# Kernel optimization log

Measured on AMD Instinct MI355X. Metric: run time of the kernel, lower is better.

The kernel has to match this reference:

```python
import jax, jax.numpy as jnp
import numpy as np

D, H, FF, EPS = 1024, 16, 4096, 1e-5

def _ln(x, g, b):
    m = jnp.mean(x, axis=-1, keepdims=True)
    v = jnp.var(x, axis=-1, keepdims=True)
    return (x - m) * jax.lax.rsqrt(v + EPS) * g + b

def setup_inputs() -> dict:
    key = jax.random.key(0)
    ks = jax.random.split(key, 8)
    b, t = 2, 2048
    return {
        "x": jax.random.normal(ks[0], (b, t, D), jnp.float32),
        "prev_attn": jax.random.normal(ks[1], (b, H, t, t), jnp.float32) * 0.1,
        "w_qkv": jax.random.normal(ks[2], (D, 3 * D), jnp.float32) * (D ** -0.5),
        "w_out": jax.random.normal(ks[3], (D, D), jnp.float32) * (D ** -0.5),
        "w1": jax.random.normal(ks[4], (D, FF), jnp.float32) * (D ** -0.5),
        "b1": jnp.zeros((FF,), jnp.float32),
        "w2": jax.random.normal(ks[5], (FF, D), jnp.float32) * (FF ** -0.5),
        "b2": jnp.zeros((D,), jnp.float32),
        "g1": jnp.ones((D,), jnp.float32),
        "be1": jnp.zeros((D,), jnp.float32),
        "g2": jnp.ones((D,), jnp.float32),
        "be2": jnp.zeros((D,), jnp.float32),
    }

def reference(x, prev_attn, w_qkv, w_out, w1, b1, w2, b2, g1, be1, g2, be2):
    b, t, d = x.shape
    h, hd = H, d // H
    scale = hd ** -0.5
    qkv = _ln(x, g1, be1) @ w_qkv                       # [b,t,3d]
    q, k, v = jnp.split(qkv, 3, axis=-1)
    q, k, v = [z.reshape(b, t, h, hd).transpose(0, 2, 1, 3) for z in (q, k, v)]
    attn = jnp.einsum('bhid,bhjd->bhij', q, k) * scale + prev_attn
    attn = jax.nn.softmax(attn, axis=-1)                # [b,h,t,t]
    out = jnp.einsum('bhij,bhjd->bhid', attn, v).transpose(0, 2, 1, 3).reshape(b, t, d)
    x = x + out @ w_out
    hdn = _ln(x, g2, be2)
    ffn = jax.nn.gelu(hdn @ w1 + b1, approximate=False) @ w2 + b2
    x = x + ffn
    return (x, jax.lax.stop_gradient(attn))
```

## Files before the change

### kernel.cpp

```cpp
#include <hip/hip_runtime.h>
#include <hip/hip_bf16.h>
#include <math.h>

#define T_SEQ 2048
#define D_MODEL 1024
#define N_HEADS 16
#define HD 64
#define FF_DIM 4096
#define N_ROWS 4096
#define LDQKV 3072

typedef __bf16 bf16x8 __attribute__((ext_vector_type(8)));
typedef float f32x4 __attribute__((ext_vector_type(4)));

__device__ __forceinline__ unsigned short f2bf(float f) {
  union { float f; unsigned u; } v; v.f = f;
  unsigned r = v.u + 0x7FFFu + ((v.u >> 16) & 1u);
  return (unsigned short)(r >> 16);
}
__device__ __forceinline__ float bf2f(unsigned short u) {
  union { unsigned u; float f; } v; v.u = ((unsigned)u) << 16;
  return v.f;
}

__device__ __forceinline__ void gld_lds16(const void* g, void* l) {
  __builtin_amdgcn_global_load_lds(
      (const __attribute__((address_space(1))) unsigned int*)g,
      (__attribute__((address_space(3))) unsigned int*)l, 16, 0, 0);
}

__global__ __launch_bounds__(256) void transpose_w(const float* __restrict__ src,
                                                   unsigned short* __restrict__ dst,
                                                   int R, int C) {
  __shared__ float tile[32][33];
  int c0 = blockIdx.x * 32, r0 = blockIdx.y * 32;
  int tx = threadIdx.x & 31, ty = threadIdx.x >> 5;
#pragma unroll
  for (int i = 0; i < 32; i += 8)
    tile[ty + i][tx] = src[(size_t)(r0 + ty + i) * C + c0 + tx];
  __syncthreads();
#pragma unroll
  for (int i = 0; i < 32; i += 8)
    dst[(size_t)(c0 + ty + i) * R + r0 + tx] = f2bf(tile[tx][ty + i]);
}

__global__ __launch_bounds__(256) void ln_kernel(const float* __restrict__ x,
                                                 const float* __restrict__ g,
                                                 const float* __restrict__ be,
                                                 unsigned short* __restrict__ out) {
  int row = blockIdx.x;
  float4 v = ((const float4*)(x + (size_t)row * D_MODEL))[threadIdx.x];
  float s = v.x + v.y + v.z + v.w;
  float ss = v.x * v.x + v.y * v.y + v.z * v.z + v.w * v.w;
#pragma unroll
  for (int o = 32; o; o >>= 1) { s += __shfl_down(s, o); ss += __shfl_down(ss, o); }
  __shared__ float red[8];
  int wid = threadIdx.x >> 6, lane = threadIdx.x & 63;
  if (lane == 0) { red[wid] = s; red[4 + wid] = ss; }
  __syncthreads();
  if (threadIdx.x == 0) {
    float S0 = red[0] + red[1] + red[2] + red[3];
    float S1 = red[4] + red[5] + red[6] + red[7];
    float m = S0 * (1.0f / D_MODEL);
    red[0] = m;
    red[1] = rsqrtf(S1 * (1.0f / D_MODEL) - m * m + 1e-5f);
  }
  __syncthreads();
  float m = red[0], inv = red[1];
  float4 gv = ((const float4*)g)[threadIdx.x];
  float4 bv = ((const float4*)be)[threadIdx.x];
  ushort4 o;
  o.x = f2bf((v.x - m) * inv * gv.x + bv.x);
  o.y = f2bf((v.y - m) * inv * gv.y + bv.y);
  o.z = f2bf((v.z - m) * inv * gv.z + bv.z);
  o.w = f2bf((v.w - m) * inv * gv.w + bv.w);
  ((ushort4*)(out + (size_t)row * D_MODEL))[threadIdx.x] = o;
}

template <int EPI>
__global__ __launch_bounds__(256) void gemm_bt(const unsigned short* __restrict__ A,
                                               const unsigned short* __restrict__ Bt,
                                               int M, int N, int K,
                                               void* __restrict__ outp,
                                               const float* __restrict__ bias,
                                               const float* __restrict__ res) {
  __shared__ __align__(16) unsigned short As[128 * 32];
  __shared__ __align__(16) unsigned short Bs[128 * 32];
  int tid = threadIdx.x;
  int m0 = blockIdx.x * 128, n0 = blockIdx.y * 128;
  int w = tid >> 6, l = tid & 63;
  int wm = w >> 1, wn = w & 1;
  int lr = l & 15, lg = l >> 4;
  f32x4 acc[4][4] = {};
  const unsigned short* ap0 = A + (size_t)(m0 + (tid >> 2)) * K + (tid & 3) * 8;
  const unsigned short* ap1 = ap0 + (size_t)64 * K;
  const unsigned short* bp0 = Bt + (size_t)(n0 + (tid >> 2)) * K + (tid & 3) * 8;
  const unsigned short* bp1 = bp0 + (size_t)64 * K;
  unsigned short* la0 = As + (tid & ~63) * 8;
  unsigned short* la1 = As + (256 + (tid & ~63)) * 8;
  unsigned short* lb0 = Bs + (tid & ~63) * 8;
  unsigned short* lb1 = Bs + (256 + (tid & ~63)) * 8;
  for (int k0 = 0; k0 < K; k0 += 32) {
    gld_lds16(ap0, la0);
    gld_lds16(ap1, la1);
    gld_lds16(bp0, lb0);
    gld_lds16(bp1, lb1);
    ap0 += 32; ap1 += 32; bp0 += 32; bp1 += 32;
    __syncthreads();
    bf16x8 af[4], bfr[4];
#pragma unroll
    for (int i = 0; i < 4; i++) {
      af[i] = *(const bf16x8*)(As + (wm * 64 + i * 16 + lr) * 32 + lg * 8);
      bfr[i] = *(const bf16x8*)(Bs + (wn * 64 + i * 16 + lr) * 32 + lg * 8);
    }
#pragma unroll
    for (int i = 0; i < 4; i++)
#pragma unroll
      for (int j = 0; j < 4; j++)
        acc[i][j] = __builtin_amdgcn_mfma_f32_16x16x32_bf16(af[i], bfr[j], acc[i][j], 0, 0, 0);
    __syncthreads();
  }
#pragma unroll
  for (int i = 0; i < 4; i++) {
#pragma unroll
    for (int j = 0; j < 4; j++) {
      int col = n0 + wn * 64 + j * 16 + lr;
#pragma unroll
      for (int r = 0; r < 4; r++) {
        int row = m0 + wm * 64 + i * 16 + lg * 4 + r;
        size_t idx = (size_t)row * N + col;
        float v = acc[i][j][r];
        if (EPI == 0) {
          if (col < 1024) v *= 0.125f;
          ((unsigned short*)outp)[idx] = f2bf(v);
        } else if (EPI == 2) {
          float t = v + bias[col];
          ((unsigned short*)outp)[idx] = f2bf(0.5f * t * (1.0f + erff(t * 0.70710678f)));
        }
      }
    }
  }
}

template <int EPI>
__global__ __launch_bounds__(256) void gemm_bt2(const unsigned short* __restrict__ A,
                                                const unsigned short* __restrict__ Bt,
                                                int M, int N, int K,
                                                void* __restrict__ outp,
                                                const float* __restrict__ bias,
                                                const float* __restrict__ res) {
  __shared__ __align__(16) unsigned short As[64 * 64];
  __shared__ __align__(16) unsigned short Bs[128 * 64];
  int tid = threadIdx.x;
  int m0 = blockIdx.x * 64, n0 = blockIdx.y * 128;
  int w = tid >> 6, l = tid & 63;
  int lr = l & 15, lg = l >> 4;
  f32x4 acc[4][2] = {};
  int srow = tid >> 3;
  int scolb = ((tid & 7) * 16) ^ ((srow & 7) << 4);
  const unsigned short* apg = A + (size_t)(m0 + srow) * K + (scolb >> 1);
  const unsigned short* bpg = Bt + (size_t)(n0 + srow) * K + (scolb >> 1);
  unsigned short* la = As + tid * 8;
  unsigned short* lb = Bs + tid * 8;
  for (int k0 = 0; k0 < K; k0 += 64) {
    gld_lds16(apg + k0, la);
    gld_lds16(apg + (size_t)32 * K + k0, la + 32 * 64);
    gld_lds16(bpg + k0, lb);
    gld_lds16(bpg + (size_t)32 * K + k0, lb + 32 * 64);
    gld_lds16(bpg + (size_t)64 * K + k0, lb + 64 * 64);
    gld_lds16(bpg + (size_t)96 * K + k0, lb + 96 * 64);
    __syncthreads();
#pragma unroll
    for (int kk = 0; kk < 2; kk++) {
      int cb = (lg * 16 + kk * 64) ^ ((lr & 7) << 4);
      bf16x8 af[4], bfr[2];
#pragma unroll
      for (int i = 0; i < 4; i++)
        af[i] = *(const bf16x8*)((const char*)As + (i * 16 + lr) * 128 + cb);
#pragma unroll
      for (int j = 0; j < 2; j++)
        bfr[j] = *(const bf16x8*)((const char*)Bs + (w * 32 + j * 16 + lr) * 128 + cb);
#pragma unroll
      for (int i = 0; i < 4; i++)
#pragma unroll
        for (int j = 0; j < 2; j++)
          acc[i][j] = __builtin_amdgcn_mfma_f32_16x16x32_bf16(af[i], bfr[j], acc[i][j], 0, 0, 0);
    }
    __syncthreads();
  }
#pragma unroll
  for (int i = 0; i < 4; i++) {
#pragma unroll
    for (int j = 0; j < 2; j++) {
      int col = n0 + w * 32 + j * 16 + lr;
#pragma unroll
      for (int r = 0; r < 4; r++) {
        int row = m0 + i * 16 + lg * 4 + r;
        size_t idx = (size_t)row * N + col;
        float v = acc[i][j][r];
        if (EPI == 1) {
          ((float*)outp)[idx] = res[idx] + v;
        } else {
          ((float*)outp)[idx] = v + bias[col] + res[idx];
        }
      }
    }
  }
}

__global__ __launch_bounds__(256) void repack_kv(const unsigned short* __restrict__ qkv,
                                                 unsigned short* __restrict__ kt,
                                                 unsigned short* __restrict__ vt2) {
  __shared__ unsigned short tile[64][66];
  int bh = blockIdx.x >> 5, tt = blockIdx.x & 31;
  int b = bh >> 4, h = bh & 15;
  int t0 = tt * 64;
  int tid = threadIdx.x;
  const unsigned short* ksrc = qkv + (size_t)(b * T_SEQ + t0) * LDQKV + D_MODEL + h * HD;
  unsigned short* kdst = kt + ((size_t)bh * T_SEQ + t0) * HD;
#pragma unroll
  for (int i = 0; i < 16; i++) {
    int e = i * 256 + tid;
    int tr = e >> 6, d = e & 63;
    kdst[(size_t)tr * HD + d] = ksrc[(size_t)tr * LDQKV + d];
  }
  const unsigned short* vsrc = qkv + (size_t)(b * T_SEQ + t0) * LDQKV + 2 * D_MODEL + h * HD;
#pragma unroll
  for (int i = 0; i < 16; i++) {
    int e = i * 256 + tid;
    int tr = e >> 6, d = e & 63;
    tile[tr][d] = vsrc[(size_t)tr * LDQKV + d];
  }
  __syncthreads();
  unsigned short* vdst = vt2 + (size_t)bh * 64 * HD * 32 + (size_t)(t0 >> 5) * HD * 32;
#pragma unroll
  for (int i = 0; i < 16; i++) {
    int e = i * 256 + tid;
    int d = e >> 6, tr = e & 63;
    vdst[(size_t)((tr >> 5) * HD + d) * 32 + (tr & 31)] = tile[tr][d];
  }
}

__global__ __launch_bounds__(512, 4) void attn_kernel(const unsigned short* __restrict__ qkv,
                                                      const unsigned short* __restrict__ kt,
                                                      const unsigned short* __restrict__ vt2,
                                                      const float* __restrict__ prev,
                                                      float* __restrict__ attn_out,
                                                      unsigned short* __restrict__ ctx) {
  __shared__ __align__(16) unsigned short S[16 * 2048];
  int bid = blockIdx.x;
  int nb = (bid & 7) * 512 + (bid >> 3);
  int bh = nb >> 7, rt = nb & 127;
  int b = bh >> 4, h = bh & 15;
  int r0 = rt * 16;
  int tid = threadIdx.x, w = tid >> 6, l = tid & 63;
  int lr = l & 15, lg = l >> 4;

  const unsigned short* qb = qkv + (size_t)(b * T_SEQ + r0 + lr) * LDQKV + h * HD + lg * 8;
  bf16x8 qf0 = *(const bf16x8*)(qb);
  bf16x8 qf1 = *(const bf16x8*)(qb + 32);

  const unsigned short* kb0 = kt + (size_t)bh * T_SEQ * HD + lg * 8;
#pragma unroll
  for (int nt = 0; nt < 16; nt++) {
    int c = w * 256 + nt * 16 + lr;
    const unsigned short* kp = kb0 + (size_t)c * HD;
    bf16x8 kf0 = *(const bf16x8*)(kp);
    bf16x8 kf1 = *(const bf16x8*)(kp + 32);
    f32x4 a = {};
    __builtin_amdgcn_s_setprio(1);
    a = __builtin_amdgcn_mfma_f32_16x16x32_bf16(qf0, kf0, a, 0, 0, 0);
    a = __builtin_amdgcn_mfma_f32_16x16x32_bf16(qf1, kf1, a, 0, 0, 0);
    __builtin_amdgcn_s_setprio(0);
#pragma unroll
    for (int r = 0; r < 4; r++) {
      int row = lg * 4 + r;
      int byteoff = (c * 2) ^ ((row & 7) << 4);
      *(unsigned short*)((char*)S + row * 4096 + byteoff) = f2bf(a[r]);
    }
  }
  __syncthreads();

  const float* pvb = prev + ((size_t)bh * T_SEQ + r0 + 2 * w) * T_SEQ;
  float* arow0 = attn_out + ((size_t)bh * T_SEQ + r0 + 2 * w) * T_SEQ;
#pragma unroll
  for (int rr = 0; rr < 2; rr++) {
    int row = w * 2 + rr;
    char* Sr = (char*)S + row * 4096;
    int xv = (row & 7) << 4;
    const float* pr = pvb + (size_t)rr * T_SEQ;
    float* ar = arow0 + (size_t)rr * T_SEQ;
    f32x4 sv[8];
    float mx = -1e30f;
#pragma unroll
    for (int i = 0; i < 8; i++) {
      int c = l * 4 + i * 256;
      ushort4 sraw = *(const ushort4*)(Sr + ((2 * c) ^ xv));
      f32x4 p = *(const f32x4*)(pr + c);
      sv[i][0] = bf2f(sraw.x) + p[0];
      sv[i][1] = bf2f(sraw.y) + p[1];
      sv[i][2] = bf2f(sraw.z) + p[2];
      sv[i][3] = bf2f(sraw.w) + p[3];
      mx = fmaxf(mx, fmaxf(fmaxf(sv[i][0], sv[i][1]), fmaxf(sv[i][2], sv[i][3])));
    }
#pragma unroll
    for (int o = 32; o; o >>= 1) mx = fmaxf(mx, __shfl_xor(mx, o));
    float sum = 0.f;
#pragma unroll
    for (int i = 0; i < 8; i++) {
      sv[i][0] = __expf(sv[i][0] - mx);
      sv[i][1] = __expf(sv[i][1] - mx);
      sv[i][2] = __expf(sv[i][2] - mx);
      sv[i][3] = __expf(sv[i][3] - mx);
      sum += sv[i][0] + sv[i][1] + sv[i][2] + sv[i][3];
    }
#pragma unroll
    for (int o = 32; o; o >>= 1) sum += __shfl_xor(sum, o);
    float inv = 1.0f / sum;
#pragma unroll
    for (int i = 0; i < 8; i++) {
      int c = l * 4 + i * 256;
      float4 p4;
      p4.x = sv[i][0] * inv; p4.y = sv[i][1] * inv;
      p4.z = sv[i][2] * inv; p4.w = sv[i][3] * inv;
      *(float4*)(ar + c) = p4;
      ushort4 pbf;
      pbf.x = f2bf(p4.x); pbf.y = f2bf(p4.y); pbf.z = f2bf(p4.z); pbf.w = f2bf(p4.w);
      *(ushort4*)(Sr + ((2 * c) ^ xv)) = pbf;
    }
  }
  __syncthreads();

  f32x4 pacc[4] = {};
  const unsigned short* vb = vt2 + (size_t)bh * 64 * HD * 32;
#pragma unroll
  for (int kt_i = 0; kt_i < 8; kt_i++) {
    int kb = w * 256 + kt_i * 32;
    char* Sr = (char*)S + lr * 4096;
    int byteoff = ((kb + lg * 8) * 2) ^ ((lr & 7) << 4);
    bf16x8 af = *(const bf16x8*)(Sr + byteoff);
    const unsigned short* vtile = vb + (size_t)(kb >> 5) * HD * 32;
    __builtin_amdgcn_s_setprio(1);
#pragma unroll
    for (int nj = 0; nj < 4; nj++) {
      const unsigned short* vp = vtile + (size_t)(nj * 16 + lr) * 32 + lg * 8;
      bf16x8 bv = *(const bf16x8*)(vp);
      pacc[nj] = __builtin_amdgcn_mfma_f32_16x16x32_bf16(af, bv, pacc[nj], 0, 0, 0);
    }
    __builtin_amdgcn_s_setprio(0);
  }
  __syncthreads();

  float* P = (float*)S;
#pragma unroll
  for (int nj = 0; nj < 4; nj++)
#pragma unroll
    for (int r = 0; r < 4; r++)
      P[(w * 16 + lg * 4 + r) * 64 + nj * 16 + lr] = pacc[nj][r];
  __syncthreads();
  for (int e = tid; e < 1024; e += 512) {
    float s = 0.f;
#pragma unroll
    for (int ww = 0; ww < 8; ww++) s += P[ww * 1024 + e];
    int row = e >> 6, col = e & 63;
    ctx[(size_t)(b * T_SEQ + r0 + row) * D_MODEL + h * HD + col] = f2bf(s);
  }
}

extern "C" void kernel_launch(void* const* d_in, const int* in_sizes, int n_in,
                              void* d_out, int out_size, void* d_ws, size_t ws_size,
                              hipStream_t stream) {
  const float* x = (const float*)d_in[0];
  const float* prev = (const float*)d_in[1];
  const float* w_qkv = (const float*)d_in[2];
  const float* w_out = (const float*)d_in[3];
  const float* w1 = (const float*)d_in[4];
  const float* b1 = (const float*)d_in[5];
  const float* w2 = (const float*)d_in[6];
  const float* b2 = (const float*)d_in[7];
  const float* g1 = (const float*)d_in[8];
  const float* be1 = (const float*)d_in[9];
  const float* g2 = (const float*)d_in[10];
  const float* be2 = (const float*)d_in[11];
  float* out_x = (float*)d_out;
  float* out_attn = out_x + (size_t)N_ROWS * D_MODEL;

  char* p = (char*)d_ws;
  auto alloc = [&](size_t bytes) -> void* {
    void* r = (void*)p;
    p += (bytes + 255) & ~(size_t)255;
    return r;
  };
  unsigned short* wqkvT = (unsigned short*)alloc((size_t)3072 * 1024 * 2);
  unsigned short* woutT = (unsigned short*)alloc((size_t)1024 * 1024 * 2);
  unsigned short* w1T   = (unsigned short*)alloc((size_t)4096 * 1024 * 2);
  unsigned short* w2T   = (unsigned short*)alloc((size_t)1024 * 4096 * 2);
  unsigned short* ln1b  = (unsigned short*)alloc((size_t)N_ROWS * 1024 * 2);
  unsigned short* qkvb  = (unsigned short*)alloc((size_t)N_ROWS * 3072 * 2);
  unsigned short* ktb   = (unsigned short*)alloc((size_t)32 * 2048 * 64 * 2);
  unsigned short* vt2b  = (unsigned short*)alloc((size_t)32 * 64 * 64 * 32 * 2);
  unsigned short* ctxb  = (unsigned short*)alloc((size_t)N_ROWS * 1024 * 2);
  float*          x2b   = (float*)alloc((size_t)N_ROWS * 1024 * 4);
  unsigned short* ln2b  = (unsigned short*)alloc((size_t)N_ROWS * 1024 * 2);
  unsigned short* hb    = (unsigned short*)alloc((size_t)N_ROWS * 4096 * 2);

  transpose_w<<<dim3(3072 / 32, 1024 / 32), 256, 0, stream>>>(w_qkv, wqkvT, 1024, 3072);
  transpose_w<<<dim3(1024 / 32, 1024 / 32), 256, 0, stream>>>(w_out, woutT, 1024, 1024);
  transpose_w<<<dim3(4096 / 32, 1024 / 32), 256, 0, stream>>>(w1, w1T, 1024, 4096);
  transpose_w<<<dim3(1024 / 32, 4096 / 32), 256, 0, stream>>>(w2, w2T, 4096, 1024);

  ln_kernel<<<N_ROWS, 256, 0, stream>>>(x, g1, be1, ln1b);
  gemm_bt<0><<<dim3(32, 24), 256, 0, stream>>>(ln1b, wqkvT, N_ROWS, 3072, 1024, qkvb, nullptr, nullptr);
  repack_kv<<<32 * 32, 256, 0, stream>>>(qkvb, ktb, vt2b);
  attn_kernel<<<32 * 128, 512, 0, stream>>>(qkvb, ktb, vt2b, prev, out_attn, ctxb);
  gemm_bt2<1><<<dim3(64, 8), 256, 0, stream>>>(ctxb, woutT, N_ROWS, 1024, 1024, x2b, nullptr, x);
  ln_kernel<<<N_ROWS, 256, 0, stream>>>(x2b, g2, be2, ln2b);
  gemm_bt<2><<<dim3(32, 32), 256, 0, stream>>>(ln2b, w1T, N_ROWS, 4096, 1024, hb, b1, nullptr);
  gemm_bt2<3><<<dim3(64, 8), 256, 0, stream>>>(hb, w2T, N_ROWS, 1024, 4096, out_x, b2, x2b);
}
```

Measured before the change: 587.1 us.

## Make attention kernel persistent over 8 query tiles with double-buffered score LDS

Each block now handles 8 consecutive 16-row query tiles of one head instead of a single tile, and the grid drops from 4096 to 512 blocks. Two LDS score buffers let the QK^T stage for tile j+2 be issued after tile j's softmax and PV stages. The PV stage now splits the 2048-long key dimension into two halves across waves, replacing the 8-way LDS reduction with a 2-way one. LDS use grows to about 136 KB per block and launch bounds fall to 1 block per CU, so latency hiding rests on the in-block staging rather than on multiple resident blocks.

```diff
diff --git a/kernel.cpp b/kernel.cpp
--- a/kernel.cpp
+++ b/kernel.cpp
@@ -9,6 +9,7 @@
 #define FF_DIM 4096
 #define N_ROWS 4096
 #define LDQKV 3072
+#define TILES 8
 
 typedef __bf16 bf16x8 __attribute__((ext_vector_type(8)));
 typedef float f32x4 __attribute__((ext_vector_type(4)));
@@ -241,129 +242,138 @@
   }
 }
 
-__global__ __launch_bounds__(512, 4) void attn_kernel(const unsigned short* __restrict__ qkv,
+__global__ __launch_bounds__(512, 1) void attn_kernel(const unsigned short* __restrict__ qkv,
                                                       const unsigned short* __restrict__ kt,
                                                       const unsigned short* __restrict__ vt2,
                                                       const float* __restrict__ prev,
                                                       float* __restrict__ attn_out,
                                                       unsigned short* __restrict__ ctx) {
-  __shared__ __align__(16) unsigned short S[16 * 2048];
+  __shared__ __align__(16) unsigned short S[2 * 16 * 2048];
+  __shared__ float red[2 * 16 * 64];
   int bid = blockIdx.x;
-  int nb = (bid & 7) * 512 + (bid >> 3);
-  int bh = nb >> 7, rt = nb & 127;
+  int bh = bid & 31;
+  int s  = bid >> 5;
   int b = bh >> 4, h = bh & 15;
-  int r0 = rt * 16;
   int tid = threadIdx.x, w = tid >> 6, l = tid & 63;
   int lr = l & 15, lg = l >> 4;
-
-  const unsigned short* qb = qkv + (size_t)(b * T_SEQ + r0 + lr) * LDQKV + h * HD + lg * 8;
-  bf16x8 qf0 = *(const bf16x8*)(qb);
-  bf16x8 qf1 = *(const bf16x8*)(qb + 32);
+  int tbase = s * TILES;
 
   const unsigned short* kb0 = kt + (size_t)bh * T_SEQ * HD + lg * 8;
-#pragma unroll
-  for (int nt = 0; nt < 16; nt++) {
-    int c = w * 256 + nt * 16 + lr;
-    const unsigned short* kp = kb0 + (size_t)c * HD;
-    bf16x8 kf0 = *(const bf16x8*)(kp);
-    bf16x8 kf1 = *(const bf16x8*)(kp + 32);
-    f32x4 a = {};
-    __builtin_amdgcn_s_setprio(1);
-    a = __builtin_amdgcn_mfma_f32_16x16x32_bf16(qf0, kf0, a, 0, 0, 0);
-    a = __builtin_amdgcn_mfma_f32_16x16x32_bf16(qf1, kf1, a, 0, 0, 0);
-    __builtin_amdgcn_s_setprio(0);
-#pragma unroll
-    for (int r = 0; r < 4; r++) {
-      int row = lg * 4 + r;
-      int byteoff = (c * 2) ^ ((row & 7) << 4);
-      *(unsigned short*)((char*)S + row * 4096 + byteoff) = f2bf(a[r]);
-    }
-  }
+  const unsigned short* vb = vt2 + (size_t)bh * 64 * HD * 32;
+
+  auto stageA = [&](int t, int buf) {
+    int r0 = t * 16;
+    const unsigned short* qb = qkv + (size_t)(b * T_SEQ + r0 + lr) * LDQKV + h * HD + lg * 8;
+    bf16x8 qf0 = *(const bf16x8*)(qb);
+    bf16x8 qf1 = *(const bf16x8*)(qb + 32);
+    char* Sb = (char*)S + buf * 65536;
+#pragma unroll
+    for (int nt = 0; nt < 16; nt++) {
+      int c = w * 256 + nt * 16 + lr;
+      const unsigned short* kp = kb0 + (size_t)c * HD;
+      bf16x8 kf0 = *(const bf16x8*)(kp);
+      bf16x8 kf1 = *(const bf16x8*)(kp + 32);
+      f32x4 a = {};
+      __builtin_amdgcn_s_setprio(1);
+      a = __builtin_amdgcn_mfma_f32_16x16x32_bf16(qf0, kf0, a, 0, 0, 0);
+      a = __builtin_amdgcn_mfma_f32_16x16x32_bf16(qf1, kf1, a, 0, 0, 0);
+      __builtin_amdgcn_s_setprio(0);
+#pragma unroll
+      for (int r = 0; r < 4; r++) {
+        int row = lg * 4 + r;
+        *(unsigned short*)(Sb + row * 4096 + ((c * 2) ^ ((row & 7) << 4))) = f2bf(a[r]);
+      }
+    }
+  };
+
+  auto stageB = [&](int t, int buf) {
+    int r0 = t * 16;
+    char* Sb = (char*)S + buf * 65536;
+    const float* pvb = prev + ((size_t)bh * T_SEQ + r0 + 2 * w) * T_SEQ;
+    float* arow0 = attn_out + ((size_t)bh * T_SEQ + r0 + 2 * w) * T_SEQ;
+#pragma unroll
+    for (int rr = 0; rr < 2; rr++) {
+      int row = w * 2 + rr;
+      char* Sr = Sb + row * 4096;
+      int xv = (row & 7) << 4;
+      const float* pr = pvb + (size_t)rr * T_SEQ;
+      float* ar = arow0 + (size_t)rr * T_SEQ;
+      f32x4 sv[8];
+      float mx = -1e30f;
+#pragma unroll
+      for (int i = 0; i < 8; i++) {
+        int c = l * 4 + i * 256;
+        ushort4 sraw = *(const ushort4*)(Sr + ((2 * c) ^ xv));
+        f32x4 p = *(const f32x4*)(pr + c);
+        sv[i][0] = bf2f(sraw.x) + p[0];
+        sv[i][1] = bf2f(sraw.y) + p[1];
+        sv[i][2] = bf2f(sraw.z) + p[2];
+        sv[i][3] = bf2f(sraw.w) + p[3];
+        mx = fmaxf(mx, fmaxf(fmaxf(sv[i][0], sv[i][1]), fmaxf(sv[i][2], sv[i][3])));
+      }
+#pragma unroll
+      for (int o = 32; o; o >>= 1) mx = fmaxf(mx, __shfl_xor(mx, o));
+      float sum = 0.f;
+#pragma unroll
+      for (int i = 0; i < 8; i++) {
+        sv[i][0] = __expf(sv[i][0] - mx);
+        sv[i][1] = __expf(sv[i][1] - mx);
+        sv[i][2] = __expf(sv[i][2] - mx);
+        sv[i][3] = __expf(sv[i][3] - mx);
+        sum += sv[i][0] + sv[i][1] + sv[i][2] + sv[i][3];
+      }
+#pragma unroll
+      for (int o = 32; o; o >>= 1) sum += __shfl_xor(sum, o);
+      float inv = 1.0f / sum;
+#pragma unroll
+      for (int i = 0; i < 8; i++) {
+        int c = l * 4 + i * 256;
+        float4 p4;
+        p4.x = sv[i][0] * inv; p4.y = sv[i][1] * inv;
+        p4.z = sv[i][2] * inv; p4.w = sv[i][3] * inv;
+        *(float4*)(ar + c) = p4;
+        ushort4 pbf;
+        pbf.x = f2bf(p4.x); pbf.y = f2bf(p4.y); pbf.z = f2bf(p4.z); pbf.w = f2bf(p4.w);
+        *(ushort4*)(Sr + ((2 * c) ^ xv)) = pbf;
+      }
+    }
+  };
+
+  auto stageC = [&](int buf) {
+    int ks = w >> 2, dq = w & 3;
+    char* Sb = (char*)S + buf * 65536;
+    f32x4 pacc = {};
+#pragma unroll
+    for (int kt_i = 0; kt_i < 32; kt_i++) {
+      int kb = ks * 1024 + kt_i * 32;
+      bf16x8 af = *(const bf16x8*)(Sb + lr * 4096 + (((kb + lg * 8) * 2) ^ ((lr & 7) << 4)));
+      const unsigned short* vp = vb + (size_t)(kb >> 5) * HD * 32 + (dq * 16 + lr) * 32 + lg * 8;
+      bf16x8 bv = *(const bf16x8*)(vp);
+      __builtin_amdgcn_s_setprio(1);
+      pacc = __builtin_amdgcn_mfma_f32_16x16x32_bf16(af, bv, pacc, 0, 0, 0);
+      __builtin_amdgcn_s_setprio(0);
+    }
+#pragma unroll
+    for (int r = 0; r < 4; r++)
+      red[ks * 1024 + (lg * 4 + r) * 64 + dq * 16 + lr] = pacc[r];
+  };
+
+  stageA(tbase + 0, 0);
+  stageA(tbase + 1, 1);
   __syncthreads();
-
-  const float* pvb = prev + ((size_t)bh * T_SEQ + r0 + 2 * w) * T_SEQ;
-  float* arow0 = attn_out + ((size_t)bh * T_SEQ + r0 + 2 * w) * T_SEQ;
-#pragma unroll
-  for (int rr = 0; rr < 2; rr++) {
-    int row = w * 2 + rr;
-    char* Sr = (char*)S + row * 4096;
-    int xv = (row & 7) << 4;
-    const float* pr = pvb + (size_t)rr * T_SEQ;
-    float* ar = arow0 + (size_t)rr * T_SEQ;
-    f32x4 sv[8];
-    float mx = -1e30f;
-#pragma unroll
-    for (int i = 0; i < 8; i++) {
-      int c = l * 4 + i * 256;
-      ushort4 sraw = *(const ushort4*)(Sr + ((2 * c) ^ xv));
-      f32x4 p = *(const f32x4*)(pr + c);
-      sv[i][0] = bf2f(sraw.x) + p[0];
-      sv[i][1] = bf2f(sraw.y) + p[1];
-      sv[i][2] = bf2f(sraw.z) + p[2];
-      sv[i][3] = bf2f(sraw.w) + p[3];
-      mx = fmaxf(mx, fmaxf(fmaxf(sv[i][0], sv[i][1]), fmaxf(sv[i][2], sv[i][3])));
-    }
-#pragma unroll
-    for (int o = 32; o; o >>= 1) mx = fmaxf(mx, __shfl_xor(mx, o));
-    float sum = 0.f;
-#pragma unroll
-    for (int i = 0; i < 8; i++) {
-      sv[i][0] = __expf(sv[i][0] - mx);
-      sv[i][1] = __expf(sv[i][1] - mx);
-      sv[i][2] = __expf(sv[i][2] - mx);
-      sv[i][3] = __expf(sv[i][3] - mx);
-      sum += sv[i][0] + sv[i][1] + sv[i][2] + sv[i][3];
-    }
-#pragma unroll
-    for (int o = 32; o; o >>= 1) sum += __shfl_xor(sum, o);
-    float inv = 1.0f / sum;
-#pragma unroll
-    for (int i = 0; i < 8; i++) {
-      int c = l * 4 + i * 256;
-      float4 p4;
-      p4.x = sv[i][0] * inv; p4.y = sv[i][1] * inv;
-      p4.z = sv[i][2] * inv; p4.w = sv[i][3] * inv;
-      *(float4*)(ar + c) = p4;
-      ushort4 pbf;
-      pbf.x = f2bf(p4.x); pbf.y = f2bf(p4.y); pbf.z = f2bf(p4.z); pbf.w = f2bf(p4.w);
-      *(ushort4*)(Sr + ((2 * c) ^ xv)) = pbf;
-    }
-  }
-  __syncthreads();
-
-  f32x4 pacc[4] = {};
-  const unsigned short* vb = vt2 + (size_t)bh * 64 * HD * 32;
-#pragma unroll
-  for (int kt_i = 0; kt_i < 8; kt_i++) {
-    int kb = w * 256 + kt_i * 32;
-    char* Sr = (char*)S + lr * 4096;
-    int byteoff = ((kb + lg * 8) * 2) ^ ((lr & 7) << 4);
-    bf16x8 af = *(const bf16x8*)(Sr + byteoff);
-    const unsigned short* vtile = vb + (size_t)(kb >> 5) * HD * 32;
-    __builtin_amdgcn_s_setprio(1);
-#pragma unroll
-    for (int nj = 0; nj < 4; nj++) {
-      const unsigned short* vp = vtile + (size_t)(nj * 16 + lr) * 32 + lg * 8;
-      bf16x8 bv = *(const bf16x8*)(vp);
-      pacc[nj] = __builtin_amdgcn_mfma_f32_16x16x32_bf16(af, bv, pacc[nj], 0, 0, 0);
-    }
-    __builtin_amdgcn_s_setprio(0);
-  }
-  __syncthreads();
-
-  float* P = (float*)S;
-#pragma unroll
-  for (int nj = 0; nj < 4; nj++)
-#pragma unroll
-    for (int r = 0; r < 4; r++)
-      P[(w * 16 + lg * 4 + r) * 64 + nj * 16 + lr] = pacc[nj][r];
-  __syncthreads();
-  for (int e = tid; e < 1024; e += 512) {
-    float s = 0.f;
-#pragma unroll
-    for (int ww = 0; ww < 8; ww++) s += P[ww * 1024 + e];
-    int row = e >> 6, col = e & 63;
-    ctx[(size_t)(b * T_SEQ + r0 + row) * D_MODEL + h * HD + col] = f2bf(s);
+  for (int j = 0; j < TILES; j++) {
+    int cur = j & 1;
+    stageB(tbase + j, cur);
+    __syncthreads();
+    stageC(cur);
+    __syncthreads();
+    int r0 = (tbase + j) * 16;
+    for (int e = tid; e < 1024; e += 512) {
+      int q = e >> 6, d = e & 63;
+      ctx[(size_t)(b * T_SEQ + r0 + q) * D_MODEL + h * HD + d] =
+          f2bf(red[q * 64 + d] + red[1024 + q * 64 + d]);
+    }
+    if (j + 2 < TILES) stageA(tbase + j + 2, cur);
   }
 }
 
@@ -412,7 +422,7 @@
   ln_kernel<<<N_ROWS, 256, 0, stream>>>(x, g1, be1, ln1b);
   gemm_bt<0><<<dim3(32, 24), 256, 0, stream>>>(ln1b, wqkvT, N_ROWS, 3072, 1024, qkvb, nullptr, nullptr);
   repack_kv<<<32 * 32, 256, 0, stream>>>(qkvb, ktb, vt2b);
-  attn_kernel<<<32 * 128, 512, 0, stream>>>(qkvb, ktb, vt2b, prev, out_attn, ctxb);
+  attn_kernel<<<512, 512, 0, stream>>>(qkvb, ktb, vt2b, prev, out_attn, ctxb);
   gemm_bt2<1><<<dim3(64, 8), 256, 0, stream>>>(ctxb, woutT, N_ROWS, 1024, 1024, x2b, nullptr, x);
   ln_kernel<<<N_ROWS, 256, 0, stream>>>(x2b, g2, be2, ln2b);
   gemm_bt<2><<<dim3(32, 32), 256, 0, stream>>>(ln2b, w1T, N_ROWS, 4096, 1024, hb, b1, nullptr);
```

Measured after the change: 897.4 us. 1.53x slower.
